# Performance work log

Measured on AMD Instinct MI355X. Metric: run time of the kernel, lower is better.

Reference implementation:

```python
import jax, jax.numpy as jnp
import numpy as np

B, N, DIM, H, DH, EDGE_DIM = 2, 320, 512, 8, 64, 64
INNER = H * DH  # 512


def setup_inputs() -> dict:
    key = jax.random.key(0)
    ks = jax.random.split(key, 8)
    s = jnp.float32(0.02)
    f32 = jnp.float32
    return {
        "nodes": jax.random.normal(ks[0], (B, N, DIM), f32),
        "edges": jax.random.normal(ks[1], (B, EDGE_DIM, N, N), f32),
        "W_exp": jax.random.normal(ks[2], (DIM, INNER), f32) * s,
        "b_exp": jnp.zeros((INNER,), f32),
        "W_q": jax.random.normal(ks[3], (INNER, INNER), f32) * s,
        "b_q": jnp.zeros((INNER,), f32),
        "W_kv": jax.random.normal(ks[4], (INNER, 2 * INNER), f32) * s,
        "b_kv": jnp.zeros((2 * INNER,), f32),
        "W_e": jax.random.normal(ks[5], (EDGE_DIM, INNER), f32) * s,
        "b_e": jnp.zeros((INNER,), f32),
        "W_out": jax.random.normal(ks[6], (INNER, DIM), f32) * s,
        "b_out": jnp.zeros((DIM,), f32),
    }


def reference(nodes, edges, W_exp, b_exp, W_q, b_q, W_kv, b_kv, W_e, b_e, W_out, b_out):
    b, n, _ = nodes.shape
    h, dh = H, DH
    scale = dh ** -0.5

    x = nodes @ W_exp + b_exp                      # [b, n, inner]
    q = x @ W_q + b_q                              # [b, n, inner]
    kv = x @ W_kv + b_kv
    k, v = jnp.split(kv, 2, axis=-1)               # each [b, n, inner]

    def split_heads(t):
        return t.reshape(b, n, h, dh).transpose(0, 2, 1, 3)  # [b, h, n, dh]

    q, k, v = map(split_heads, (q, k, v))

    # edges: [b, edge_dim, i, j] -> projected edge k/v bias [b, h, i, j, dh]
    e = jnp.einsum('beij,ed->bijd', edges, W_e) + b_e
    e = e.reshape(b, n, n, h, dh).transpose(0, 3, 1, 2, 4)

    # sim = q . (k + e); split into matmul term + edge term (same math)
    sim = (jnp.einsum('bhid,bhjd->bhij', q, k)
           + jnp.einsum('bhid,bhijd->bhij', q, e)) * scale
    attn = jax.nn.softmax(sim, axis=-1)            # [b, h, i, j]

    # out = attn . (v + e)
    out = (jnp.einsum('bhij,bhjd->bhid', attn, v)
           + jnp.einsum('bhij,bhijd->bhid', attn, e))
    out = out.transpose(0, 2, 1, 3).reshape(b, n, h * dh)  # [b, n, inner]
    return out @ W_out + b_out
```

## Files before the change

kernel.cpp:

```cpp
#include <hip/hip_runtime.h>

#define B_  2
#define N_  320
#define H_  8
#define ED_ 64

typedef __attribute__((ext_vector_type(8))) short bf16x8;
typedef __attribute__((ext_vector_type(4))) float floatx4;

__device__ __forceinline__ ushort f2bf(float f) {
    union { float f; unsigned u; } c; c.f = f;
    unsigned u = c.u;
    return (ushort)((u + 0x7fffu + ((u >> 16) & 1u)) >> 16);
}
__device__ __forceinline__ float bf2f(ushort s) {
    union { unsigned u; float f; } c; c.u = ((unsigned)s) << 16;
    return c.f;
}
__device__ __forceinline__ uint4 packf8(const float* f) {
    uint4 r;
    r.x = (unsigned)f2bf(f[0]) | ((unsigned)f2bf(f[1]) << 16);
    r.y = (unsigned)f2bf(f[2]) | ((unsigned)f2bf(f[3]) << 16);
    r.z = (unsigned)f2bf(f[4]) | ((unsigned)f2bf(f[5]) << 16);
    r.w = (unsigned)f2bf(f[6]) | ((unsigned)f2bf(f[7]) << 16);
    return r;
}
__device__ __forceinline__ uint4 packu8(const ushort* s) {
    uint4 r;
    r.x = (unsigned)s[0] | ((unsigned)s[1] << 16);
    r.y = (unsigned)s[2] | ((unsigned)s[3] << 16);
    r.z = (unsigned)s[4] | ((unsigned)s[5] << 16);
    r.w = (unsigned)s[6] | ((unsigned)s[7] << 16);
    return r;
}

__global__ __launch_bounds__(256) void prep_kernel(
    const float* __restrict__ W_exp, const float* __restrict__ W_q,
    const float* __restrict__ W_kv, const float* __restrict__ W_out,
    const float* __restrict__ W_e, const float* __restrict__ nodes,
    ushort* __restrict__ WT_exp, ushort* __restrict__ WT_qkv,
    ushort* __restrict__ WT_oh, ushort* __restrict__ WT_ol,
    float* __restrict__ W_eT, ushort* __restrict__ nodes_bf)
{
    __shared__ float T[64][65];
    const int id = blockIdx.x, tid = threadIdx.x;

    if (id >= 328) {
        long base = (long)(id - 328) * 4096 + (long)tid * 16;
        float f[16];
        #pragma unroll
        for (int e = 0; e < 4; ++e) {
            float4 x4 = *(const float4*)&nodes[base + e * 4];
            f[e*4] = x4.x; f[e*4+1] = x4.y; f[e*4+2] = x4.z; f[e*4+3] = x4.w;
        }
        uint4 p0 = packf8(f), p1 = packf8(f + 8);
        *(uint4*)&nodes_bf[base] = p0;
        *(uint4*)&nodes_bf[base + 8] = p1;
        return;
    }
    if (id >= 320) {
        const int c0 = (id - 320) * 64;
        const int r = tid >> 2, cs = (tid & 3) * 16;
        #pragma unroll
        for (int e = 0; e < 4; ++e) {
            float4 x4 = *(const float4*)&W_e[(long)r * 512 + c0 + cs + e * 4];
            T[r][cs + e*4] = x4.x; T[r][cs + e*4 + 1] = x4.y;
            T[r][cs + e*4 + 2] = x4.z; T[r][cs + e*4 + 3] = x4.w;
        }
        __syncthreads();
        const int hd = c0 + (tid >> 2), ks = (tid & 3) * 16;
        #pragma unroll
        for (int e = 0; e < 4; ++e) {
            float4 o4;
            o4.x = T[ks + e*4][tid >> 2];     o4.y = T[ks + e*4 + 1][tid >> 2];
            o4.z = T[ks + e*4 + 2][tid >> 2]; o4.w = T[ks + e*4 + 3][tid >> 2];
            *(float4*)&W_eT[(long)hd * 64 + ks + e * 4] = o4;
        }
        return;
    }
    const float* src; ushort* dst; ushort* dstl = nullptr;
    int ldS, row0, kt, ct;
    if (id < 64)       { int l = id;       kt = l >> 3; ct = l & 7;  src = W_exp; ldS = 512;  dst = WT_exp; row0 = ct * 64; }
    else if (id < 128) { int l = id - 64;  kt = l >> 3; ct = l & 7;  src = W_q;   ldS = 512;  dst = WT_qkv; row0 = ct * 64; }
    else if (id < 256) { int l = id - 128; kt = l >> 4; ct = l & 15; src = W_kv;  ldS = 1024; dst = WT_qkv; row0 = 512 + ct * 64; }
    else               { int l = id - 256; kt = l >> 3; ct = l & 7;  src = W_out; ldS = 512;  dst = WT_oh; dstl = WT_ol; row0 = ct * 64; }
    const int k0 = kt * 64, c0 = ct * 64;
    {
        const int r = tid >> 2, cs = (tid & 3) * 16;
        #pragma unroll
        for (int e = 0; e < 4; ++e) {
            float4 x4 = *(const float4*)&src[(long)(k0 + r) * ldS + c0 + cs + e * 4];
            T[r][cs + e*4] = x4.x; T[r][cs + e*4 + 1] = x4.y;
            T[r][cs + e*4 + 2] = x4.z; T[r][cs + e*4 + 3] = x4.w;
        }
    }
    __syncthreads();
    {
        const int cc = tid >> 2, ks = (tid & 3) * 16;
        float vals[16];
        #pragma unroll
        for (int e = 0; e < 16; ++e) vals[e] = T[ks + e][cc];
        ushort* d = dst + (long)(row0 + cc) * 512 + k0 + ks;
        if (!dstl) {
            *(uint4*)d = packf8(vals);
            *(uint4*)(d + 8) = packf8(vals + 8);
        } else {
            ushort hs[16], ls[16];
            #pragma unroll
            for (int e = 0; e < 16; ++e) {
                hs[e] = f2bf(vals[e]);
                ls[e] = f2bf(vals[e] - bf2f(hs[e]));
            }
            *(uint4*)d = packu8(hs);
            *(uint4*)(d + 8) = packu8(hs + 8);
            ushort* d2 = dstl + (long)(row0 + cc) * 512 + k0 + ks;
            *(uint4*)d2 = packu8(ls);
            *(uint4*)(d2 + 8) = packu8(ls + 8);
        }
    }
}

template <int MODE>
__global__ __launch_bounds__(256) void gemm_v2(
    const ushort* __restrict__ A, const ushort* __restrict__ WT,
    const float* __restrict__ bias1, const float* __restrict__ bias2,
    ushort* __restrict__ outbf, float* __restrict__ q_o,
    float* __restrict__ kt_o, float* __restrict__ v_o)
{
    __shared__ ushort As[64 * 64];
    __shared__ ushort Bs[64 * 64];
    const int tid = threadIdx.x, lane = tid & 63, wid = tid >> 6;
    const int wr = wid >> 1, wc = wid & 1;
    const int bm = blockIdx.x * 64, bn = blockIdx.y * 64;
    const int srow = tid >> 2, sk = tid & 3;
    const int sw = (srow & 7) << 4;
    const int d1 = srow * 128 + ((sk * 32) ^ sw);
    const int d2 = srow * 128 + ((sk * 32 + 16) ^ sw);
    const ushort* Asrc = A + (long)(bm + srow) * 512 + sk * 16;
    const ushort* Bsrc = WT + (long)(bn + srow) * 512 + sk * 16;

    floatx4 acc[2][2] = {};
    for (int k0 = 0; k0 < 512; k0 += 64) {
        uint4 a0 = *(const uint4*)(Asrc + k0);
        uint4 a1 = *(const uint4*)(Asrc + k0 + 8);
        uint4 b0 = *(const uint4*)(Bsrc + k0);
        uint4 b1 = *(const uint4*)(Bsrc + k0 + 8);
        if (k0) __syncthreads();
        *(uint4*)((char*)As + d1) = a0;
        *(uint4*)((char*)As + d2) = a1;
        *(uint4*)((char*)Bs + d1) = b0;
        *(uint4*)((char*)Bs + d2) = b1;
        __syncthreads();
        #pragma unroll
        for (int s = 0; s < 2; ++s) {
            const int kb = s * 64 + ((lane >> 4) * 16);
            bf16x8 af[2], bfr[2];
            #pragma unroll
            for (int mf = 0; mf < 2; ++mf) {
                int row = wr * 32 + mf * 16 + (lane & 15);
                af[mf] = *(const bf16x8*)((const char*)As + row * 128 + (kb ^ ((row & 7) << 4)));
            }
            #pragma unroll
            for (int nf = 0; nf < 2; ++nf) {
                int col = wc * 32 + nf * 16 + (lane & 15);
                bfr[nf] = *(const bf16x8*)((const char*)Bs + col * 128 + (kb ^ ((col & 7) << 4)));
            }
            #pragma unroll
            for (int mf = 0; mf < 2; ++mf)
                #pragma unroll
                for (int nf = 0; nf < 2; ++nf)
                    acc[mf][nf] = __builtin_amdgcn_mfma_f32_16x16x32_bf16(
                        af[mf], bfr[nf], acc[mf][nf], 0, 0, 0);
        }
    }
    const int r4 = (lane >> 4) * 4, c16 = lane & 15;
    #pragma unroll
    for (int mf = 0; mf < 2; ++mf)
        #pragma unroll
        for (int nf = 0; nf < 2; ++nf)
            #pragma unroll
            for (int j = 0; j < 4; ++j) {
                int row = bm + wr * 32 + mf * 16 + r4 + j;
                int cn  = bn + wc * 32 + nf * 16 + c16;
                float val = acc[mf][nf][j];
                if (MODE == 0) {
                    outbf[(long)row * 512 + cn] = f2bf(val + bias1[cn]);
                } else {
                    if (cn < 512) {
                        q_o[(long)row * 512 + cn] = val + bias1[cn];
                    } else if (cn < 1024) {
                        int bb = row / N_, ii = row % N_;
                        kt_o[((long)bb * 512 + (cn - 512)) * N_ + ii] = val + bias2[cn - 512];
                    } else {
                        v_o[(long)row * 512 + (cn - 1024)] = val + bias2[cn - 512];
                    }
                }
            }
}

__global__ __launch_bounds__(256) void gemm_out(
    const float* __restrict__ Af, const ushort* __restrict__ BTh,
    const ushort* __restrict__ BTl, const float* __restrict__ bias,
    float* __restrict__ C)
{
    __shared__ ushort Ah[64 * 64], Al[64 * 64], Bh[64 * 64], Bl[64 * 64];
    const int tid = threadIdx.x, lane = tid & 63, wid = tid >> 6;
    const int wr = wid >> 1, wc = wid & 1;
    const int bm = blockIdx.x * 64, bn = blockIdx.y * 64;
    const int srow = tid >> 2, sk = tid & 3;
    const int sw = (srow & 7) << 4;
    const int d1 = srow * 128 + ((sk * 32) ^ sw);
    const int d2 = srow * 128 + ((sk * 32 + 16) ^ sw);
    const float*  asrc = Af + (long)(bm + srow) * 512 + sk * 16;
    const ushort* bhs  = BTh + (long)(bn + srow) * 512 + sk * 16;
    const ushort* bls  = BTl + (long)(bn + srow) * 512 + sk * 16;

    floatx4 acc[2][2] = {};
    for (int k0 = 0; k0 < 512; k0 += 64) {
        float f[16];
        #pragma unroll
        for (int e = 0; e < 4; ++e) {
            float4 x4 = *(const float4*)(asrc + k0 + e * 4);
            f[e*4] = x4.x; f[e*4+1] = x4.y; f[e*4+2] = x4.z; f[e*4+3] = x4.w;
        }
        ushort hs[16], ls[16];
        #pragma unroll
        for (int e = 0; e < 16; ++e) {
            hs[e] = f2bf(f[e]);
            ls[e] = f2bf(f[e] - bf2f(hs[e]));
        }
        uint4 bh0 = *(const uint4*)(bhs + k0);
        uint4 bh1 = *(const uint4*)(bhs + k0 + 8);
        uint4 bl0 = *(const uint4*)(bls + k0);
        uint4 bl1 = *(const uint4*)(bls + k0 + 8);
        if (k0) __syncthreads();
        *(uint4*)((char*)Ah + d1) = packu8(hs);
        *(uint4*)((char*)Ah + d2) = packu8(hs + 8);
        *(uint4*)((char*)Al + d1) = packu8(ls);
        *(uint4*)((char*)Al + d2) = packu8(ls + 8);
        *(uint4*)((char*)Bh + d1) = bh0;
        *(uint4*)((char*)Bh + d2) = bh1;
        *(uint4*)((char*)Bl + d1) = bl0;
        *(uint4*)((char*)Bl + d2) = bl1;
        __syncthreads();
        #pragma unroll
        for (int s = 0; s < 2; ++s) {
            const int kb = s * 64 + ((lane >> 4) * 16);
            bf16x8 ah[2], al[2], bh[2], bl[2];
            #pragma unroll
            for (int mf = 0; mf < 2; ++mf) {
                int row = wr * 32 + mf * 16 + (lane & 15);
                int off = row * 128 + (kb ^ ((row & 7) << 4));
                ah[mf] = *(const bf16x8*)((const char*)Ah + off);
                al[mf] = *(const bf16x8*)((const char*)Al + off);
            }
            #pragma unroll
            for (int nf = 0; nf < 2; ++nf) {
                int col = wc * 32 + nf * 16 + (lane & 15);
                int off = col * 128 + (kb ^ ((col & 7) << 4));
                bh[nf] = *(const bf16x8*)((const char*)Bh + off);
                bl[nf] = *(const bf16x8*)((const char*)Bl + off);
            }
            #pragma unroll
            for (int mf = 0; mf < 2; ++mf)
                #pragma unroll
                for (int nf = 0; nf < 2; ++nf) {
                    acc[mf][nf] = __builtin_amdgcn_mfma_f32_16x16x32_bf16(ah[mf], bh[nf], acc[mf][nf], 0, 0, 0);
                    acc[mf][nf] = __builtin_amdgcn_mfma_f32_16x16x32_bf16(ah[mf], bl[nf], acc[mf][nf], 0, 0, 0);
                    acc[mf][nf] = __builtin_amdgcn_mfma_f32_16x16x32_bf16(al[mf], bh[nf], acc[mf][nf], 0, 0, 0);
                }
        }
    }
    const int r4 = (lane >> 4) * 4, c16 = lane & 15;
    #pragma unroll
    for (int mf = 0; mf < 2; ++mf)
        #pragma unroll
        for (int nf = 0; nf < 2; ++nf)
            #pragma unroll
            for (int j = 0; j < 4; ++j) {
                int row = bm + wr * 32 + mf * 16 + r4 + j;
                int col = bn + wc * 32 + nf * 16 + c16;
                C[(long)row * 512 + col] = acc[mf][nf][j] + bias[col];
            }
}

__global__ __launch_bounds__(512) void attn_kernel(
    const float* __restrict__ q, const float* __restrict__ k_t,
    const float* __restrict__ v, const float* __restrict__ edges,
    const float* __restrict__ W_eT, const float* __restrict__ W_e,
    const float* __restrict__ b_e, float* __restrict__ o_out)
{
    __shared__ ushort E_s[64 * 324];
    __shared__ ushort A_bf[8 * 320];
    __shared__ float  q_lds[512];
    __shared__ float  tu_lds[512];

    const int blk = blockIdx.x;
    const int b = blk / N_, i = blk % N_;
    const int tid = threadIdx.x;
    const int w = tid >> 6, lane = tid & 63;

    q_lds[tid] = q[(long)blk * 512 + tid];
    {
        const float* ebase = edges + (long)b * ED_ * N_ * N_ + (long)i * N_;
        for (int idx = tid; idx < 64 * 160; idx += 512) {
            int c = idx / 160, jj = (idx % 160) * 2;
            float2 e2 = *(const float2*)(ebase + (long)c * (N_ * N_) + jj);
            unsigned lo = f2bf(e2.x), hi = f2bf(e2.y);
            *(unsigned*)&E_s[c * 324 + jj] = lo | (hi << 16);
        }
    }
    __syncthreads();

    {
        float tacc = 0.f;
        const float* we = W_eT + (long)(w * 64) * 64 + lane;
        const float* ql = q_lds + w * 64;
        #pragma unroll 8
        for (int d = 0; d < 64; ++d) tacc += ql[d] * we[(long)d * 64];
        tu_lds[tid] = tacc;
    }
    __syncthreads();

    float sacc[5] = {0.f, 0.f, 0.f, 0.f, 0.f};
    {
        const float* tl = tu_lds + w * 64;
        #pragma unroll 4
        for (int c = 0; c < 64; ++c) {
            float tc = tl[c];
            const ushort* er = &E_s[c * 324 + lane];
            sacc[0] += tc * bf2f(er[0]);
            sacc[1] += tc * bf2f(er[64]);
            sacc[2] += tc * bf2f(er[128]);
            sacc[3] += tc * bf2f(er[192]);
            sacc[4] += tc * bf2f(er[256]);
        }
        const float* ql = q_lds + w * 64;
        const float* kb = k_t + ((long)b * 512 + w * 64) * N_;
        #pragma unroll 4
        for (int d = 0; d < 64; ++d) {
            float qd = ql[d];
            const float* kr = kb + (long)d * N_ + lane;
            sacc[0] += qd * kr[0];
            sacc[1] += qd * kr[64];
            sacc[2] += qd * kr[128];
            sacc[3] += qd * kr[192];
            sacc[4] += qd * kr[256];
        }
    }
    const float scale = 0.125f;
    float s0 = sacc[0] * scale, s1 = sacc[1] * scale, s2 = sacc[2] * scale,
          s3 = sacc[3] * scale, s4 = sacc[4] * scale;

    float m = fmaxf(fmaxf(fmaxf(s0, s1), fmaxf(s2, s3)), s4);
    #pragma unroll
    for (int off = 32; off >= 1; off >>= 1) m = fmaxf(m, __shfl_xor(m, off, 64));
    s0 = __expf(s0 - m); s1 = __expf(s1 - m); s2 = __expf(s2 - m);
    s3 = __expf(s3 - m); s4 = __expf(s4 - m);
    float sum = s0 + s1 + s2 + s3 + s4;
    #pragma unroll
    for (int off = 32; off >= 1; off >>= 1) sum += __shfl_xor(sum, off, 64);
    float inv = 1.f / sum;
    A_bf[w * 320 + lane]       = f2bf(s0 * inv);
    A_bf[w * 320 + 64 + lane]  = f2bf(s1 * inv);
    A_bf[w * 320 + 128 + lane] = f2bf(s2 * inv);
    A_bf[w * 320 + 192 + lane] = f2bf(s3 * inv);
    A_bf[w * 320 + 256 + lane] = f2bf(s4 * inv);
    __syncthreads();

    float acc_v = 0.f, acc_u = 0.f;
    {
        const float*  vb = v + (long)b * N_ * 512 + w * 64 + lane;
        const ushort* Er = E_s + lane * 324;
        const ushort* Ar = A_bf + w * 320;
        #pragma unroll 4
        for (int j4 = 0; j4 < 80; ++j4) {
            uint2 aa = *(const uint2*)&Ar[j4 * 4];
            float a0 = bf2f((ushort)(aa.x & 0xffffu));
            float a1 = bf2f((ushort)(aa.x >> 16));
            float a2 = bf2f((ushort)(aa.y & 0xffffu));
            float a3 = bf2f((ushort)(aa.y >> 16));
            uint2 e2 = *(const uint2*)&Er[j4 * 4];
            float e0 = bf2f((ushort)(e2.x & 0xffffu));
            float e1 = bf2f((ushort)(e2.x >> 16));
            float e2f = bf2f((ushort)(e2.y & 0xffffu));
            float e3 = bf2f((ushort)(e2.y >> 16));
            const float* vv = vb + (long)j4 * 4 * 512;
            acc_v += a0 * vv[0] + a1 * vv[512] + a2 * vv[1024] + a3 * vv[1536];
            acc_u += a0 * e0 + a1 * e1 + a2 * e2f + a3 * e3;
        }
    }
    tu_lds[tid] = acc_u;
    __syncthreads();

    float o_val = acc_v + b_e[w * 64 + lane];
    {
        const float* wb = W_e + w * 64 + lane;
        const float* Ur = tu_lds + w * 64;
        #pragma unroll 8
        for (int c = 0; c < 64; ++c)
            o_val += Ur[c] * wb[(long)c * 512];
    }
    o_out[(long)blk * 512 + w * 64 + lane] = o_val;
}

extern "C" void kernel_launch(void* const* d_in, const int* in_sizes, int n_in,
                              void* d_out, int out_size, void* d_ws, size_t ws_size,
                              hipStream_t stream)
{
    const float* nodes = (const float*)d_in[0];
    const float* edges = (const float*)d_in[1];
    const float* W_exp = (const float*)d_in[2];
    const float* b_exp = (const float*)d_in[3];
    const float* W_q   = (const float*)d_in[4];
    const float* b_q   = (const float*)d_in[5];
    const float* W_kv  = (const float*)d_in[6];
    const float* b_kv  = (const float*)d_in[7];
    const float* W_e   = (const float*)d_in[8];
    const float* b_e   = (const float*)d_in[9];
    const float* W_out = (const float*)d_in[10];
    const float* b_out = (const float*)d_in[11];
    float* out = (float*)d_out;

    const long SZ = (long)B_ * N_ * 512;
    float* ws  = (float*)d_ws;
    float* q   = ws;
    float* k_t = ws + SZ;
    float* v   = ws + 2 * SZ;
    float* o   = ws + 3 * SZ;
    ushort* x_bf     = (ushort*)(ws + 4 * SZ);
    ushort* nodes_bf = x_bf + SZ;
    ushort* WT_exp   = nodes_bf + SZ;
    ushort* WT_qkv   = WT_exp + 262144;
    ushort* WT_oh    = WT_qkv + 786432;
    ushort* WT_ol    = WT_oh + 262144;
    float*  W_eT     = (float*)(WT_ol + 262144);

    prep_kernel<<<408, 256, 0, stream>>>(W_exp, W_q, W_kv, W_out, W_e, nodes,
                                         WT_exp, WT_qkv, WT_oh, WT_ol, W_eT, nodes_bf);
    gemm_v2<0><<<dim3(10, 8), 256, 0, stream>>>(nodes_bf, WT_exp, b_exp, nullptr,
                                                x_bf, nullptr, nullptr, nullptr);
    gemm_v2<1><<<dim3(10, 24), 256, 0, stream>>>(x_bf, WT_qkv, b_q, b_kv,
                                                 nullptr, q, k_t, v);
    attn_kernel<<<640, 512, 0, stream>>>(q, k_t, v, edges, W_eT, W_e, b_e, o);
    gemm_out<<<dim3(10, 8), 256, 0, stream>>>(o, WT_oh, WT_ol, b_out, out);
}
```

Before: 178.7 us.

## Split attention into MFMA QK, softmax/edge kernel, and MFMA AV+edge-projection kernels

Moves the q·k score computation and the attn·v plus edge-value projection out of the per-row scalar attention kernel into separate tiled MFMA kernels. They use bf16 hi/lo splits for precision and the per-row kernel keeps only the edge term, softmax and the attn·E reduction. The nodes bf16 conversion is folded into the first GEMM, and v is written transposed for the new AV kernel. This replaces strided scalar global reads of k and v with matrix-core work, at the cost of two extra launches and round-trips of the full score and attention matrices through global memory.

```diff
diff --git a/kernel.cpp b/kernel.cpp
--- a/kernel.cpp
+++ b/kernel.cpp
@@ -37,27 +37,14 @@
 __global__ __launch_bounds__(256) void prep_kernel(
     const float* __restrict__ W_exp, const float* __restrict__ W_q,
     const float* __restrict__ W_kv, const float* __restrict__ W_out,
-    const float* __restrict__ W_e, const float* __restrict__ nodes,
+    const float* __restrict__ W_e,
     ushort* __restrict__ WT_exp, ushort* __restrict__ WT_qkv,
     ushort* __restrict__ WT_oh, ushort* __restrict__ WT_ol,
-    float* __restrict__ W_eT, ushort* __restrict__ nodes_bf)
+    float* __restrict__ W_eT, ushort* __restrict__ Wehi, ushort* __restrict__ Welo)
 {
     __shared__ float T[64][65];
     const int id = blockIdx.x, tid = threadIdx.x;
 
-    if (id >= 328) {
-        long base = (long)(id - 328) * 4096 + (long)tid * 16;
-        float f[16];
-        #pragma unroll
-        for (int e = 0; e < 4; ++e) {
-            float4 x4 = *(const float4*)&nodes[base + e * 4];
-            f[e*4] = x4.x; f[e*4+1] = x4.y; f[e*4+2] = x4.z; f[e*4+3] = x4.w;
-        }
-        uint4 p0 = packf8(f), p1 = packf8(f + 8);
-        *(uint4*)&nodes_bf[base] = p0;
-        *(uint4*)&nodes_bf[base + 8] = p1;
-        return;
-    }
     if (id >= 320) {
         const int c0 = (id - 320) * 64;
         const int r = tid >> 2, cs = (tid & 3) * 16;
@@ -68,14 +55,24 @@
             T[r][cs + e*4 + 2] = x4.z; T[r][cs + e*4 + 3] = x4.w;
         }
         __syncthreads();
-        const int hd = c0 + (tid >> 2), ks = (tid & 3) * 16;
+        const int cc = tid >> 2, ks = (tid & 3) * 16;
+        const int hd = c0 + cc;
+        float vals[16]; ushort hs[16], ls[16];
+        #pragma unroll
+        for (int e = 0; e < 16; ++e) {
+            vals[e] = T[ks + e][cc];
+            hs[e] = f2bf(vals[e]);
+            ls[e] = f2bf(vals[e] - bf2f(hs[e]));
+        }
         #pragma unroll
         for (int e = 0; e < 4; ++e) {
-            float4 o4;
-            o4.x = T[ks + e*4][tid >> 2];     o4.y = T[ks + e*4 + 1][tid >> 2];
-            o4.z = T[ks + e*4 + 2][tid >> 2]; o4.w = T[ks + e*4 + 3][tid >> 2];
+            float4 o4; o4.x = vals[e*4]; o4.y = vals[e*4+1]; o4.z = vals[e*4+2]; o4.w = vals[e*4+3];
             *(float4*)&W_eT[(long)hd * 64 + ks + e * 4] = o4;
         }
+        *(uint4*)&Wehi[(long)hd * 64 + ks]     = packu8(hs);
+        *(uint4*)&Wehi[(long)hd * 64 + ks + 8] = packu8(hs + 8);
+        *(uint4*)&Welo[(long)hd * 64 + ks]     = packu8(ls);
+        *(uint4*)&Welo[(long)hd * 64 + ks + 8] = packu8(ls + 8);
         return;
     }
     const float* src; ushort* dst; ushort* dstl = nullptr;
@@ -122,13 +119,14 @@
 
 template <int MODE>
 __global__ __launch_bounds__(256) void gemm_v2(
-    const ushort* __restrict__ A, const ushort* __restrict__ WT,
+    const void* __restrict__ Asrc, const ushort* __restrict__ WT,
     const float* __restrict__ bias1, const float* __restrict__ bias2,
     ushort* __restrict__ outbf, float* __restrict__ q_o,
-    float* __restrict__ kt_o, float* __restrict__ v_o)
+    float* __restrict__ k_o, float* __restrict__ vt_o)
 {
     __shared__ ushort As[64 * 64];
     __shared__ ushort Bs[64 * 64];
+    __shared__ float  T[64][65];
     const int tid = threadIdx.x, lane = tid & 63, wid = tid >> 6;
     const int wr = wid >> 1, wc = wid & 1;
     const int bm = blockIdx.x * 64, bn = blockIdx.y * 64;
@@ -136,13 +134,24 @@
     const int sw = (srow & 7) << 4;
     const int d1 = srow * 128 + ((sk * 32) ^ sw);
     const int d2 = srow * 128 + ((sk * 32 + 16) ^ sw);
-    const ushort* Asrc = A + (long)(bm + srow) * 512 + sk * 16;
     const ushort* Bsrc = WT + (long)(bn + srow) * 512 + sk * 16;
 
     floatx4 acc[2][2] = {};
     for (int k0 = 0; k0 < 512; k0 += 64) {
-        uint4 a0 = *(const uint4*)(Asrc + k0);
-        uint4 a1 = *(const uint4*)(Asrc + k0 + 8);
+        uint4 a0, a1;
+        if (MODE == 0) {
+            const float* ap = (const float*)Asrc + (long)(bm + srow) * 512 + k0 + sk * 16;
+            float f[16];
+            #pragma unroll
+            for (int e = 0; e < 4; ++e) {
+                float4 x4 = *(const float4*)(ap + e * 4);
+                f[e*4] = x4.x; f[e*4+1] = x4.y; f[e*4+2] = x4.z; f[e*4+3] = x4.w;
+            }
+            a0 = packf8(f); a1 = packf8(f + 8);
+        } else {
+            const ushort* ap = (const ushort*)Asrc + (long)(bm + srow) * 512 + k0 + sk * 16;
+            a0 = *(const uint4*)ap; a1 = *(const uint4*)(ap + 8);
+        }
         uint4 b0 = *(const uint4*)(Bsrc + k0);
         uint4 b1 = *(const uint4*)(Bsrc + k0 + 8);
         if (k0) __syncthreads();
@@ -174,27 +183,385 @@
         }
     }
     const int r4 = (lane >> 4) * 4, c16 = lane & 15;
+    if (MODE == 0) {
+        #pragma unroll
+        for (int mf = 0; mf < 2; ++mf)
+            #pragma unroll
+            for (int nf = 0; nf < 2; ++nf)
+                #pragma unroll
+                for (int j = 0; j < 4; ++j) {
+                    int row = bm + wr * 32 + mf * 16 + r4 + j;
+                    int cn  = bn + wc * 32 + nf * 16 + c16;
+                    outbf[(long)row * 512 + cn] = f2bf(acc[mf][nf][j] + bias1[cn]);
+                }
+    } else {
+        const int cat = blockIdx.y >> 3;
+        if (cat == 0) {
+            #pragma unroll
+            for (int mf = 0; mf < 2; ++mf)
+                #pragma unroll
+                for (int nf = 0; nf < 2; ++nf)
+                    #pragma unroll
+                    for (int j = 0; j < 4; ++j) {
+                        int row = bm + wr * 32 + mf * 16 + r4 + j;
+                        int cn  = bn + wc * 32 + nf * 16 + c16;
+                        q_o[(long)row * 512 + cn] = acc[mf][nf][j] + bias1[cn];
+                    }
+        } else if (cat == 1) {
+            #pragma unroll
+            for (int mf = 0; mf < 2; ++mf)
+                #pragma unroll
+                for (int nf = 0; nf < 2; ++nf)
+                    #pragma unroll
+                    for (int j = 0; j < 4; ++j) {
+                        int row = bm + wr * 32 + mf * 16 + r4 + j;
+                        int cn  = bn + wc * 32 + nf * 16 + c16;
+                        k_o[(long)row * 512 + (cn - 512)] = acc[mf][nf][j] + bias2[cn - 512];
+                    }
+        } else {
+            #pragma unroll
+            for (int mf = 0; mf < 2; ++mf)
+                #pragma unroll
+                for (int nf = 0; nf < 2; ++nf)
+                    #pragma unroll
+                    for (int j = 0; j < 4; ++j) {
+                        int rl = wr * 32 + mf * 16 + r4 + j;
+                        int cl = wc * 32 + nf * 16 + c16;
+                        T[rl][cl] = acc[mf][nf][j] + bias2[bn - 512 + cl];
+                    }
+            __syncthreads();
+            const int cl = tid >> 2, rl4 = (tid & 3) * 16;
+            const int bb = bm / N_, ii0 = bm % N_, cv0 = bn - 1024;
+            const long orow = (long)bb * 512 + cv0 + cl;
+            #pragma unroll
+            for (int e4 = 0; e4 < 4; ++e4) {
+                float4 o4;
+                o4.x = T[rl4 + e4*4 + 0][cl]; o4.y = T[rl4 + e4*4 + 1][cl];
+                o4.z = T[rl4 + e4*4 + 2][cl]; o4.w = T[rl4 + e4*4 + 3][cl];
+                *(float4*)&vt_o[orow * N_ + ii0 + rl4 + e4*4] = o4;
+            }
+        }
+    }
+}
+
+__global__ __launch_bounds__(256) void k_qk(
+    const float* __restrict__ q, const float* __restrict__ k,
+    float* __restrict__ S_g)
+{
+    __shared__ ushort Qh[64 * 64], Ql[64 * 64], Kt[320 * 64];
+    const int it = blockIdx.x, bh = blockIdx.y;
+    const int b = bh >> 3, h = bh & 7;
+    const int tid = threadIdx.x, lane = tid & 63, wid = tid >> 6;
+    const int srow = tid >> 2, sk = tid & 3;
+    const int sw = (srow & 7) << 4;
+    const int d1 = srow * 128 + ((sk * 32) ^ sw);
+    const int d2 = srow * 128 + ((sk * 32 + 16) ^ sw);
+
+    {
+        const float* ap = q + (long)(b * N_ + it * 64 + srow) * 512 + h * 64 + sk * 16;
+        float f[16]; ushort hs[16], ls[16];
+        #pragma unroll
+        for (int e = 0; e < 4; ++e) {
+            float4 x4 = *(const float4*)(ap + e * 4);
+            f[e*4] = 0.125f * x4.x; f[e*4+1] = 0.125f * x4.y;
+            f[e*4+2] = 0.125f * x4.z; f[e*4+3] = 0.125f * x4.w;
+        }
+        #pragma unroll
+        for (int e = 0; e < 16; ++e) {
+            hs[e] = f2bf(f[e]);
+            ls[e] = f2bf(f[e] - bf2f(hs[e]));
+        }
+        *(uint4*)((char*)Qh + d1) = packu8(hs);
+        *(uint4*)((char*)Qh + d2) = packu8(hs + 8);
+        *(uint4*)((char*)Ql + d1) = packu8(ls);
+        *(uint4*)((char*)Ql + d2) = packu8(ls + 8);
+    }
+    #pragma unroll
+    for (int p = 0; p < 5; ++p) {
+        const int row = p * 64 + srow;
+        const float* kp = k + (long)(b * N_ + row) * 512 + h * 64 + sk * 16;
+        float f[16];
+        #pragma unroll
+        for (int e = 0; e < 4; ++e) {
+            float4 x4 = *(const float4*)(kp + e * 4);
+            f[e*4] = x4.x; f[e*4+1] = x4.y; f[e*4+2] = x4.z; f[e*4+3] = x4.w;
+        }
+        *(uint4*)((char*)Kt + row * 128 + ((sk * 32) ^ sw))      = packf8(f);
+        *(uint4*)((char*)Kt + row * 128 + ((sk * 32 + 16) ^ sw)) = packf8(f + 8);
+    }
+    __syncthreads();
+
+    const int j0w = wid * 80;
+    floatx4 acc[4][5] = {};
+    #pragma unroll
+    for (int s = 0; s < 2; ++s) {
+        const int kb = s * 64 + ((lane >> 4) * 16);
+        bf16x8 afh[4], afl[4], bf[5];
+        #pragma unroll
+        for (int mf = 0; mf < 4; ++mf) {
+            int row = mf * 16 + (lane & 15);
+            int off = row * 128 + (kb ^ ((row & 7) << 4));
+            afh[mf] = *(const bf16x8*)((const char*)Qh + off);
+            afl[mf] = *(const bf16x8*)((const char*)Ql + off);
+        }
+        #pragma unroll
+        for (int jt = 0; jt < 5; ++jt) {
+            int row = j0w + jt * 16 + (lane & 15);
+            bf[jt] = *(const bf16x8*)((const char*)Kt + row * 128 + (kb ^ ((row & 7) << 4)));
+        }
+        #pragma unroll
+        for (int mf = 0; mf < 4; ++mf)
+            #pragma unroll
+            for (int jt = 0; jt < 5; ++jt) {
+                acc[mf][jt] = __builtin_amdgcn_mfma_f32_16x16x32_bf16(afh[mf], bf[jt], acc[mf][jt], 0, 0, 0);
+                acc[mf][jt] = __builtin_amdgcn_mfma_f32_16x16x32_bf16(afl[mf], bf[jt], acc[mf][jt], 0, 0, 0);
+            }
+    }
+    const int r4 = (lane >> 4) * 4, c16 = lane & 15;
+    #pragma unroll
+    for (int mf = 0; mf < 4; ++mf)
+        #pragma unroll
+        for (int jt = 0; jt < 5; ++jt)
+            #pragma unroll
+            for (int e = 0; e < 4; ++e) {
+                int ri = it * 64 + mf * 16 + r4 + e;
+                int cj = j0w + jt * 16 + c16;
+                S_g[((long)bh * N_ + ri) * N_ + cj] = acc[mf][jt][e];
+            }
+}
+
+__global__ __launch_bounds__(512) void attn_kernel(
+    const float* __restrict__ q, const float* __restrict__ S_g,
+    const float* __restrict__ edges, const float* __restrict__ W_eT,
+    ushort* __restrict__ A_g, float* __restrict__ U_g)
+{
+    __shared__ ushort E_s[64 * 324];
+    __shared__ ushort A_lds[8 * 320];
+    __shared__ float  q_lds[512];
+    __shared__ float  t_lds[512];
+
+    const int blk = blockIdx.x;
+    const int b = blk / N_, i = blk % N_;
+    const int tid = threadIdx.x;
+    const int w = tid >> 6, lane = tid & 63;
+
+    q_lds[tid] = q[(long)blk * 512 + tid];
+    {
+        const float* ebase = edges + (long)b * ED_ * N_ * N_ + (long)i * N_;
+        for (int idx = tid; idx < 64 * 80; idx += 512) {
+            int c = idx / 80, j4 = (idx % 80) * 4;
+            float4 e4 = *(const float4*)(ebase + (long)c * (N_ * N_) + j4);
+            uint2 pk;
+            pk.x = (unsigned)f2bf(e4.x) | ((unsigned)f2bf(e4.y) << 16);
+            pk.y = (unsigned)f2bf(e4.z) | ((unsigned)f2bf(e4.w) << 16);
+            *(uint2*)&E_s[c * 324 + j4] = pk;
+        }
+    }
+    __syncthreads();
+
+    {
+        float tacc = 0.f;
+        const float* we = W_eT + (long)(w * 64) * 64 + lane;
+        const float* ql = q_lds + w * 64;
+        #pragma unroll 8
+        for (int d = 0; d < 64; ++d) tacc += ql[d] * we[(long)d * 64];
+        t_lds[tid] = tacc;
+    }
+    __syncthreads();
+
+    float sacc[5] = {0.f, 0.f, 0.f, 0.f, 0.f};
+    {
+        const float* tl = t_lds + w * 64;
+        #pragma unroll 4
+        for (int c = 0; c < 64; ++c) {
+            float tc = tl[c];
+            const ushort* er = &E_s[c * 324 + lane];
+            sacc[0] += tc * bf2f(er[0]);
+            sacc[1] += tc * bf2f(er[64]);
+            sacc[2] += tc * bf2f(er[128]);
+            sacc[3] += tc * bf2f(er[192]);
+            sacc[4] += tc * bf2f(er[256]);
+        }
+    }
+    const long sbase = ((long)(b * 8 + w) * N_ + i) * N_ + lane;
+    const float scale = 0.125f;
+    float s0 = sacc[0] * scale + S_g[sbase];
+    float s1 = sacc[1] * scale + S_g[sbase + 64];
+    float s2 = sacc[2] * scale + S_g[sbase + 128];
+    float s3 = sacc[3] * scale + S_g[sbase + 192];
+    float s4 = sacc[4] * scale + S_g[sbase + 256];
+
+    float m = fmaxf(fmaxf(fmaxf(s0, s1), fmaxf(s2, s3)), s4);
+    #pragma unroll
+    for (int off = 32; off >= 1; off >>= 1) m = fmaxf(m, __shfl_xor(m, off, 64));
+    s0 = __expf(s0 - m); s1 = __expf(s1 - m); s2 = __expf(s2 - m);
+    s3 = __expf(s3 - m); s4 = __expf(s4 - m);
+    float sum = s0 + s1 + s2 + s3 + s4;
+    #pragma unroll
+    for (int off = 32; off >= 1; off >>= 1) sum += __shfl_xor(sum, off, 64);
+    float inv = 1.f / sum;
+    ushort a0 = f2bf(s0 * inv), a1 = f2bf(s1 * inv), a2 = f2bf(s2 * inv),
+           a3 = f2bf(s3 * inv), a4 = f2bf(s4 * inv);
+    A_lds[w * 320 + lane]       = a0;
+    A_lds[w * 320 + 64 + lane]  = a1;
+    A_lds[w * 320 + 128 + lane] = a2;
+    A_lds[w * 320 + 192 + lane] = a3;
+    A_lds[w * 320 + 256 + lane] = a4;
+    A_g[sbase]       = a0;
+    A_g[sbase + 64]  = a1;
+    A_g[sbase + 128] = a2;
+    A_g[sbase + 192] = a3;
+    A_g[sbase + 256] = a4;
+    __syncthreads();
+
+    float acc_u = 0.f;
+    {
+        const ushort* Er = E_s + lane * 324;
+        const ushort* Ar = A_lds + w * 320;
+        #pragma unroll 4
+        for (int j4 = 0; j4 < 80; ++j4) {
+            uint2 aa = *(const uint2*)&Ar[j4 * 4];
+            uint2 e2 = *(const uint2*)&Er[j4 * 4];
+            acc_u += bf2f((ushort)(aa.x & 0xffffu)) * bf2f((ushort)(e2.x & 0xffffu));
+            acc_u += bf2f((ushort)(aa.x >> 16))     * bf2f((ushort)(e2.x >> 16));
+            acc_u += bf2f((ushort)(aa.y & 0xffffu)) * bf2f((ushort)(e2.y & 0xffffu));
+            acc_u += bf2f((ushort)(aa.y >> 16))     * bf2f((ushort)(e2.y >> 16));
+        }
+    }
+    U_g[((long)(b * 8 + w) * N_ + i) * 64 + lane] = acc_u;
+}
+
+__global__ __launch_bounds__(256) void k_ov(
+    const ushort* __restrict__ A_g, const float* __restrict__ vt,
+    const float* __restrict__ U_g, const ushort* __restrict__ Wh_g,
+    const ushort* __restrict__ Wl_g, const float* __restrict__ b_e,
+    float* __restrict__ o_out)
+{
+    __shared__ ushort B0[64 * 64], B1[64 * 64], B2[64 * 64], B3[64 * 64];
+    const int it = blockIdx.x, bh = blockIdx.y;
+    const int b = bh >> 3, h = bh & 7;
+    const int tid = threadIdx.x, lane = tid & 63, wid = tid >> 6;
+    const int wr = wid >> 1, wc = wid & 1;
+    const int srow = tid >> 2, sk = tid & 3;
+    const int sw = (srow & 7) << 4;
+    const int d1 = srow * 128 + ((sk * 32) ^ sw);
+    const int d2 = srow * 128 + ((sk * 32 + 16) ^ sw);
+
+    floatx4 acc[2][2] = {};
+    for (int j0 = 0; j0 < 320; j0 += 64) {
+        const ushort* ap = A_g + ((long)bh * N_ + it * 64 + srow) * N_ + j0 + sk * 16;
+        uint4 a0 = *(const uint4*)ap, a1 = *(const uint4*)(ap + 8);
+        const float* vp = vt + ((long)b * 512 + h * 64 + srow) * N_ + j0 + sk * 16;
+        float f[16]; ushort hs[16], ls[16];
+        #pragma unroll
+        for (int e = 0; e < 4; ++e) {
+            float4 x4 = *(const float4*)(vp + e * 4);
+            f[e*4] = x4.x; f[e*4+1] = x4.y; f[e*4+2] = x4.z; f[e*4+3] = x4.w;
+        }
+        #pragma unroll
+        for (int e = 0; e < 16; ++e) {
+            hs[e] = f2bf(f[e]);
+            ls[e] = f2bf(f[e] - bf2f(hs[e]));
+        }
+        if (j0) __syncthreads();
+        *(uint4*)((char*)B0 + d1) = a0;
+        *(uint4*)((char*)B0 + d2) = a1;
+        *(uint4*)((char*)B1 + d1) = packu8(hs);
+        *(uint4*)((char*)B1 + d2) = packu8(hs + 8);
+        *(uint4*)((char*)B2 + d1) = packu8(ls);
+        *(uint4*)((char*)B2 + d2) = packu8(ls + 8);
+        __syncthreads();
+        #pragma unroll
+        for (int s = 0; s < 2; ++s) {
+            const int kb = s * 64 + ((lane >> 4) * 16);
+            bf16x8 af[2], bh_[2], bl_[2];
+            #pragma unroll
+            for (int mf = 0; mf < 2; ++mf) {
+                int row = wr * 32 + mf * 16 + (lane & 15);
+                af[mf] = *(const bf16x8*)((const char*)B0 + row * 128 + (kb ^ ((row & 7) << 4)));
+            }
+            #pragma unroll
+            for (int nf = 0; nf < 2; ++nf) {
+                int col = wc * 32 + nf * 16 + (lane & 15);
+                int off = col * 128 + (kb ^ ((col & 7) << 4));
+                bh_[nf] = *(const bf16x8*)((const char*)B1 + off);
+                bl_[nf] = *(const bf16x8*)((const char*)B2 + off);
+            }
+            #pragma unroll
+            for (int mf = 0; mf < 2; ++mf)
+                #pragma unroll
+                for (int nf = 0; nf < 2; ++nf) {
+                    acc[mf][nf] = __builtin_amdgcn_mfma_f32_16x16x32_bf16(af[mf], bh_[nf], acc[mf][nf], 0, 0, 0);
+                    acc[mf][nf] = __builtin_amdgcn_mfma_f32_16x16x32_bf16(af[mf], bl_[nf], acc[mf][nf], 0, 0, 0);
+                }
+        }
+    }
+    {
+        const float* up = U_g + ((long)bh * N_ + it * 64 + srow) * 64 + sk * 16;
+        float f[16]; ushort uh[16], ul[16];
+        #pragma unroll
+        for (int e = 0; e < 4; ++e) {
+            float4 x4 = *(const float4*)(up + e * 4);
+            f[e*4] = x4.x; f[e*4+1] = x4.y; f[e*4+2] = x4.z; f[e*4+3] = x4.w;
+        }
+        #pragma unroll
+        for (int e = 0; e < 16; ++e) {
+            uh[e] = f2bf(f[e]);
+            ul[e] = f2bf(f[e] - bf2f(uh[e]));
+        }
+        const ushort* whp = Wh_g + ((long)h * 64 + srow) * 64 + sk * 16;
+        const ushort* wlp = Wl_g + ((long)h * 64 + srow) * 64 + sk * 16;
+        uint4 w0 = *(const uint4*)whp, w1 = *(const uint4*)(whp + 8);
+        uint4 x0 = *(const uint4*)wlp, x1 = *(const uint4*)(wlp + 8);
+        __syncthreads();
+        *(uint4*)((char*)B0 + d1) = packu8(uh);
+        *(uint4*)((char*)B0 + d2) = packu8(uh + 8);
+        *(uint4*)((char*)B1 + d1) = packu8(ul);
+        *(uint4*)((char*)B1 + d2) = packu8(ul + 8);
+        *(uint4*)((char*)B2 + d1) = w0;
+        *(uint4*)((char*)B2 + d2) = w1;
+        *(uint4*)((char*)B3 + d1) = x0;
+        *(uint4*)((char*)B3 + d2) = x1;
+        __syncthreads();
+        #pragma unroll
+        for (int s = 0; s < 2; ++s) {
+            const int kb = s * 64 + ((lane >> 4) * 16);
+            bf16x8 ah[2], al[2], wh_[2], wl_[2];
+            #pragma unroll
+            for (int mf = 0; mf < 2; ++mf) {
+                int row = wr * 32 + mf * 16 + (lane & 15);
+                int off = row * 128 + (kb ^ ((row & 7) << 4));
+                ah[mf] = *(const bf16x8*)((const char*)B0 + off);
+                al[mf] = *(const bf16x8*)((const char*)B1 + off);
+            }
+            #pragma unroll
+            for (int nf = 0; nf < 2; ++nf) {
+                int col = wc * 32 + nf * 16 + (lane & 15);
+                int off = col * 128 + (kb ^ ((col & 7) << 4));
+                wh_[nf] = *(const bf16x8*)((const char*)B2 + off);
+                wl_[nf] = *(const bf16x8*)((const char*)B3 + off);
+            }
+            #pragma unroll
+            for (int mf = 0; mf < 2; ++mf)
+                #pragma unroll
+                for (int nf = 0; nf < 2; ++nf) {
+                    acc[mf][nf] = __builtin_amdgcn_mfma_f32_16x16x32_bf16(ah[mf], wh_[nf], acc[mf][nf], 0, 0, 0);
+                    acc[mf][nf] = __builtin_amdgcn_mfma_f32_16x16x32_bf16(al[mf], wh_[nf], acc[mf][nf], 0, 0, 0);
+                    acc[mf][nf] = __builtin_amdgcn_mfma_f32_16x16x32_bf16(ah[mf], wl_[nf], acc[mf][nf], 0, 0, 0);
+                }
+        }
+    }
+    const int r4 = (lane >> 4) * 4, c16 = lane & 15;
     #pragma unroll
     for (int mf = 0; mf < 2; ++mf)
         #pragma unroll
         for (int nf = 0; nf < 2; ++nf)
             #pragma unroll
-            for (int j = 0; j < 4; ++j) {
-                int row = bm + wr * 32 + mf * 16 + r4 + j;
-                int cn  = bn + wc * 32 + nf * 16 + c16;
-                float val = acc[mf][nf][j];
-                if (MODE == 0) {
-                    outbf[(long)row * 512 + cn] = f2bf(val + bias1[cn]);
-                } else {
-                    if (cn < 512) {
-                        q_o[(long)row * 512 + cn] = val + bias1[cn];
-                    } else if (cn < 1024) {
-                        int bb = row / N_, ii = row % N_;
-                        kt_o[((long)bb * 512 + (cn - 512)) * N_ + ii] = val + bias2[cn - 512];
-                    } else {
-                        v_o[(long)row * 512 + (cn - 1024)] = val + bias2[cn - 512];
-                    }
-                }
+            for (int e = 0; e < 4; ++e) {
+                int row = it * 64 + wr * 32 + mf * 16 + r4 + e;
+                int col = wc * 32 + nf * 16 + c16;
+                o_out[((long)(b * N_ + row)) * 512 + h * 64 + col] =
+                    acc[mf][nf][e] + b_e[h * 64 + col];
             }
 }
 
@@ -282,126 +649,6 @@
                 int col = bn + wc * 32 + nf * 16 + c16;
                 C[(long)row * 512 + col] = acc[mf][nf][j] + bias[col];
             }
-}
-
-__global__ __launch_bounds__(512) void attn_kernel(
-    const float* __restrict__ q, const float* __restrict__ k_t,
-    const float* __restrict__ v, const float* __restrict__ edges,
-    const float* __restrict__ W_eT, const float* __restrict__ W_e,
-    const float* __restrict__ b_e, float* __restrict__ o_out)
-{
-    __shared__ ushort E_s[64 * 324];
-    __shared__ ushort A_bf[8 * 320];
-    __shared__ float  q_lds[512];
-    __shared__ float  tu_lds[512];
-
-    const int blk = blockIdx.x;
-    const int b = blk / N_, i = blk % N_;
-    const int tid = threadIdx.x;
-    const int w = tid >> 6, lane = tid & 63;
-
-    q_lds[tid] = q[(long)blk * 512 + tid];
-    {
-        const float* ebase = edges + (long)b * ED_ * N_ * N_ + (long)i * N_;
-        for (int idx = tid; idx < 64 * 160; idx += 512) {
-            int c = idx / 160, jj = (idx % 160) * 2;
-            float2 e2 = *(const float2*)(ebase + (long)c * (N_ * N_) + jj);
-            unsigned lo = f2bf(e2.x), hi = f2bf(e2.y);
-            *(unsigned*)&E_s[c * 324 + jj] = lo | (hi << 16);
-        }
-    }
-    __syncthreads();
-
-    {
-        float tacc = 0.f;
-        const float* we = W_eT + (long)(w * 64) * 64 + lane;
-        const float* ql = q_lds + w * 64;
-        #pragma unroll 8
-        for (int d = 0; d < 64; ++d) tacc += ql[d] * we[(long)d * 64];
-        tu_lds[tid] = tacc;
-    }
-    __syncthreads();
-
-    float sacc[5] = {0.f, 0.f, 0.f, 0.f, 0.f};
-    {
-        const float* tl = tu_lds + w * 64;
-        #pragma unroll 4
-        for (int c = 0; c < 64; ++c) {
-            float tc = tl[c];
-            const ushort* er = &E_s[c * 324 + lane];
-            sacc[0] += tc * bf2f(er[0]);
-            sacc[1] += tc * bf2f(er[64]);
-            sacc[2] += tc * bf2f(er[128]);
-            sacc[3] += tc * bf2f(er[192]);
-            sacc[4] += tc * bf2f(er[256]);
-        }
-        const float* ql = q_lds + w * 64;
-        const float* kb = k_t + ((long)b * 512 + w * 64) * N_;
-        #pragma unroll 4
-        for (int d = 0; d < 64; ++d) {
-            float qd = ql[d];
-            const float* kr = kb + (long)d * N_ + lane;
-            sacc[0] += qd * kr[0];
-            sacc[1] += qd * kr[64];
-            sacc[2] += qd * kr[128];
-            sacc[3] += qd * kr[192];
-            sacc[4] += qd * kr[256];
-        }
-    }
-    const float scale = 0.125f;
-    float s0 = sacc[0] * scale, s1 = sacc[1] * scale, s2 = sacc[2] * scale,
-          s3 = sacc[3] * scale, s4 = sacc[4] * scale;
-
-    float m = fmaxf(fmaxf(fmaxf(s0, s1), fmaxf(s2, s3)), s4);
-    #pragma unroll
-    for (int off = 32; off >= 1; off >>= 1) m = fmaxf(m, __shfl_xor(m, off, 64));
-    s0 = __expf(s0 - m); s1 = __expf(s1 - m); s2 = __expf(s2 - m);
-    s3 = __expf(s3 - m); s4 = __expf(s4 - m);
-    float sum = s0 + s1 + s2 + s3 + s4;
-    #pragma unroll
-    for (int off = 32; off >= 1; off >>= 1) sum += __shfl_xor(sum, off, 64);
-    float inv = 1.f / sum;
-    A_bf[w * 320 + lane]       = f2bf(s0 * inv);
-    A_bf[w * 320 + 64 + lane]  = f2bf(s1 * inv);
-    A_bf[w * 320 + 128 + lane] = f2bf(s2 * inv);
-    A_bf[w * 320 + 192 + lane] = f2bf(s3 * inv);
-    A_bf[w * 320 + 256 + lane] = f2bf(s4 * inv);
-    __syncthreads();
-
-    float acc_v = 0.f, acc_u = 0.f;
-    {
-        const float*  vb = v + (long)b * N_ * 512 + w * 64 + lane;
-        const ushort* Er = E_s + lane * 324;
-        const ushort* Ar = A_bf + w * 320;
-        #pragma unroll 4
-        for (int j4 = 0; j4 < 80; ++j4) {
-            uint2 aa = *(const uint2*)&Ar[j4 * 4];
-            float a0 = bf2f((ushort)(aa.x & 0xffffu));
-            float a1 = bf2f((ushort)(aa.x >> 16));
-            float a2 = bf2f((ushort)(aa.y & 0xffffu));
-            float a3 = bf2f((ushort)(aa.y >> 16));
-            uint2 e2 = *(const uint2*)&Er[j4 * 4];
-            float e0 = bf2f((ushort)(e2.x & 0xffffu));
-            float e1 = bf2f((ushort)(e2.x >> 16));
-            float e2f = bf2f((ushort)(e2.y & 0xffffu));
-            float e3 = bf2f((ushort)(e2.y >> 16));
-            const float* vv = vb + (long)j4 * 4 * 512;
-            acc_v += a0 * vv[0] + a1 * vv[512] + a2 * vv[1024] + a3 * vv[1536];
-            acc_u += a0 * e0 + a1 * e1 + a2 * e2f + a3 * e3;
-        }
-    }
-    tu_lds[tid] = acc_u;
-    __syncthreads();
-
-    float o_val = acc_v + b_e[w * 64 + lane];
-    {
-        const float* wb = W_e + w * 64 + lane;
-        const float* Ur = tu_lds + w * 64;
-        #pragma unroll 8
-        for (int c = 0; c < 64; ++c)
-            o_val += Ur[c] * wb[(long)c * 512];
-    }
-    o_out[(long)blk * 512 + w * 64 + lane] = o_val;
 }
 
 extern "C" void kernel_launch(void* const* d_in, const int* in_sizes, int n_in,
@@ -423,25 +670,32 @@
     float* out = (float*)d_out;
 
     const long SZ = (long)B_ * N_ * 512;
-    float* ws  = (float*)d_ws;
-    float* q   = ws;
-    float* k_t = ws + SZ;
-    float* v   = ws + 2 * SZ;
-    float* o   = ws + 3 * SZ;
-    ushort* x_bf     = (ushort*)(ws + 4 * SZ);
-    ushort* nodes_bf = x_bf + SZ;
-    ushort* WT_exp   = nodes_bf + SZ;
-    ushort* WT_qkv   = WT_exp + 262144;
-    ushort* WT_oh    = WT_qkv + 786432;
-    ushort* WT_ol    = WT_oh + 262144;
-    float*  W_eT     = (float*)(WT_ol + 262144);
-
-    prep_kernel<<<408, 256, 0, stream>>>(W_exp, W_q, W_kv, W_out, W_e, nodes,
-                                         WT_exp, WT_qkv, WT_oh, WT_ol, W_eT, nodes_bf);
-    gemm_v2<0><<<dim3(10, 8), 256, 0, stream>>>(nodes_bf, WT_exp, b_exp, nullptr,
+    float* ws   = (float*)d_ws;
+    float* q    = ws;
+    float* k    = ws + SZ;
+    float* v_t  = ws + 2 * SZ;
+    float* U_g  = ws + 3 * SZ;
+    float* S    = ws + 3 * SZ + 131072;
+    float* o    = S;
+    ushort* A_g    = (ushort*)(S + 1638400);
+    ushort* x_bf   = A_g + 1638400;
+    ushort* WT_exp = x_bf + SZ;
+    ushort* WT_qkv = WT_exp + 262144;
+    ushort* WT_oh  = WT_qkv + 786432;
+    ushort* WT_ol  = WT_oh + 262144;
+    float*  W_eT   = (float*)(WT_ol + 262144);
+    ushort* Wehi   = (ushort*)(W_eT + 32768);
+    ushort* Welo   = Wehi + 32768;
+
+    prep_kernel<<<328, 256, 0, stream>>>(W_exp, W_q, W_kv, W_out, W_e,
+                                         WT_exp, WT_qkv, WT_oh, WT_ol,
+                                         W_eT, Wehi, Welo);
+    gemm_v2<0><<<dim3(10, 8), 256, 0, stream>>>(nodes, WT_exp, b_exp, nullptr,
                                                 x_bf, nullptr, nullptr, nullptr);
     gemm_v2<1><<<dim3(10, 24), 256, 0, stream>>>(x_bf, WT_qkv, b_q, b_kv,
-                                                 nullptr, q, k_t, v);
-    attn_kernel<<<640, 512, 0, stream>>>(q, k_t, v, edges, W_eT, W_e, b_e, o);
+                                                 nullptr, q, k, v_t);
+    k_qk<<<dim3(5, 16), 256, 0, stream>>>(q, k, S);
+    attn_kernel<<<640, 512, 0, stream>>>(q, S, edges, W_eT, A_g, U_g);
+    k_ov<<<dim3(5, 16), 256, 0, stream>>>(A_g, v_t, U_g, Wehi, Welo, b_e, o);
     gemm_out<<<dim3(10, 8), 256, 0, stream>>>(o, WT_oh, WT_ol, b_out, out);
 }
```

New measurement: 177.2 us. Within noise of the previous version (-0.8%).
